# Kernel tuning notes

Measured on AMD Instinct MI355X. Metric: run time of the kernel, lower is better.

Reference implementation:

```python
import jax, jax.numpy as jnp
import numpy as np

B, S, D, H, F, E, TOPK, W = 1, 4096, 768, 12, 3072, 7, 2, 256  # W = one-sided window


def _layer_norm(x, g, b, eps=1e-5):
    m = jnp.mean(x, -1, keepdims=True)
    v = jnp.var(x, -1, keepdims=True)
    return (x - m) * jax.lax.rsqrt(v + eps) * g + b


def _sliding_attn(x, Wq, bq, Wk, bk, Wv, bv):
    # Longformer sliding-window attention, chunked (no dense SxS matrix).
    Bx, Sx, Dx = x.shape
    Dh = Dx // H
    def proj(Wm, bm):
        return (x @ Wm + bm).reshape(Bx, Sx, H, Dh).transpose(0, 2, 1, 3)  # [B,H,S,Dh]
    q = proj(Wq, bq) * (1.0 / np.sqrt(Dh))
    k = proj(Wk, bk)
    v = proj(Wv, bv)
    nc = Sx // W
    kp = jnp.pad(k, ((0, 0), (0, 0), (W, W), (0, 0)))
    vp = jnp.pad(v, ((0, 0), (0, 0), (W, W), (0, 0)))
    # each query chunk of W tokens sees a 3W key window
    idx = (jnp.arange(nc) * W)[:, None] + jnp.arange(3 * W)[None, :]  # [nc,3W]
    kc = kp[:, :, idx]  # [B,H,nc,3W,Dh]
    vc = vp[:, :, idx]
    qc = q.reshape(Bx, H, nc, W, Dh)
    scores = jnp.einsum('bhcqd,bhckd->bhcqk', qc, kc)  # [B,H,nc,W,3W]
    qi = jnp.arange(W)[:, None]
    ki = jnp.arange(3 * W)[None, :]
    band = (ki >= qi) & (ki <= qi + 2 * W)  # |key_pos - query_pos| <= W
    pos = (jnp.arange(nc) * W)[:, None, None] + ki[None] - W  # global key pos
    valid = band[None] & (pos >= 0) & (pos < Sx)  # [nc,W,3W]
    scores = jnp.where(valid[None, None], scores, -1e9)
    probs = jax.nn.softmax(scores, axis=-1)
    out = jnp.einsum('bhcqk,bhckd->bhcqd', probs, vc)
    return out.reshape(Bx, H, Sx, Dh).transpose(0, 2, 1, 3).reshape(Bx, Sx, Dx)


def setup_inputs() -> dict:
    key = jax.random.key(0)
    ks = jax.random.split(key, 16)
    sc = 0.02
    rn = lambda k, shp: jax.random.normal(k, shp, jnp.float32) * sc
    return {
        'hidden_states': jax.random.normal(ks[0], (B, S, D), jnp.float32),
        'Wq': rn(ks[1], (D, D)), 'bq': jnp.zeros((D,), jnp.float32),
        'Wk': rn(ks[2], (D, D)), 'bk': jnp.zeros((D,), jnp.float32),
        'Wv': rn(ks[3], (D, D)), 'bv': jnp.zeros((D,), jnp.float32),
        'Wo': rn(ks[4], (D, D)), 'bo': jnp.zeros((D,), jnp.float32),
        'ln1_g': jnp.ones((D,), jnp.float32), 'ln1_b': jnp.zeros((D,), jnp.float32),
        'gate_W': rn(ks[5], (D, E)), 'gate_b': jnp.zeros((E,), jnp.float32),
        'W1e': rn(ks[6], (E, D, F)), 'b1e': jnp.zeros((E, F), jnp.float32),
        'W2e': rn(ks[7], (E, F, D)), 'b2e': jnp.zeros((E, D), jnp.float32),
        'Wd': rn(ks[8], (D, D)), 'bd': jnp.zeros((D,), jnp.float32),
        'ln2_g': jnp.ones((D,), jnp.float32), 'ln2_b': jnp.zeros((D,), jnp.float32),
    }


def reference(hidden_states, Wq, bq, Wk, bk, Wv, bv, Wo, bo, ln1_g, ln1_b,
              gate_W, gate_b, W1e, b1e, W2e, b2e, Wd, bd, ln2_g, ln2_b):
    # attention + SelfOutput (dense + residual + LN); dropout = identity (eval)
    attn = _sliding_attn(hidden_states, Wq, bq, Wk, bk, Wv, bv)
    attention_output = _layer_norm(attn @ Wo + bo + hidden_states, ln1_g, ln1_b)
    # MoE feed-forward: dense all-experts compute, top-k masked softmax gate
    gate_logits = attention_output @ gate_W + gate_b  # [B,S,E]
    topv, topi = jax.lax.top_k(gate_logits, TOPK)
    # softmax over (-inf scatter of topk) == softmax over topk values scattered back
    sw = jax.nn.softmax(topv, axis=-1)  # [B,S,k]
    gate_weights = jnp.einsum('bske,bsk->bse',
                              jax.nn.one_hot(topi, E, dtype=attention_output.dtype), sw)
    h = jax.nn.gelu(jnp.einsum('bsd,edf->bsef', attention_output, W1e) + b1e,
                    approximate=False)  # [B,S,E,F]
    eo = jnp.einsum('bsef,efd->bsed', h, W2e) + b2e  # [B,S,E,D]
    moe = jnp.einsum('bsed,bse->bsd', eo, gate_weights)
    ffn = moe @ Wd + bd
    layer_output = _layer_norm(ffn + attention_output, ln2_g, ln2_b)
    return layer_output, gate_weights
```

## Files before the change

### kernel.cpp

```cpp
#include <hip/hip_runtime.h>
#include <math.h>

#define S_LEN 4096
#define DMODEL 768
#define NHEADS 12
#define DH 64
#define FDIM 3072
#define NEXP 7
#define NPAIR (2*S_LEN)
#define MAXTILES 40

typedef _Float16 f16x8 __attribute__((ext_vector_type(8)));
typedef float f32x4 __attribute__((ext_vector_type(4)));

__device__ __forceinline__ unsigned short f2h(float f){
  union { _Float16 h; unsigned short u; } v; v.h = (_Float16)f; return v.u;
}
__device__ __forceinline__ float gelu_f(float x){
  return 0.5f * x * (1.0f + erff(x * 0.7071067811865475f));
}
__device__ __forceinline__ f32x4 mfma16(f16x8 a, f16x8 b, f32x4 c){
  return __builtin_amdgcn_mfma_f32_16x16x32_f16(a, b, c, 0, 0, 0);
}
__device__ __forceinline__ void glds16(const void* g, void* l){
  __builtin_amdgcn_global_load_lds((const __attribute__((address_space(1))) unsigned*)g,
                                   (__attribute__((address_space(3))) unsigned*)l, 16, 0, 0);
}

__global__ __launch_bounds__(256) void split_kernel(const float* __restrict__ in,
    unsigned short* __restrict__ out, int n){
  int i = blockIdx.x*256 + threadIdx.x;
  if (i >= n) return;
  out[i] = f2h(in[i]);
}

__global__ __launch_bounds__(256) void transp_kernel(const float* __restrict__ in,
    unsigned short* __restrict__ out,
    int R, int C, long inStride, long outStride){
  const float* ip = in + (long)blockIdx.z * inStride;
  long ob = (long)blockIdx.z * outStride;
  __shared__ float tile[32][33];
  int c0 = blockIdx.x*32, r0 = blockIdx.y*32;
  int tx = threadIdx.x, ty = threadIdx.y;
  for (int i = ty; i < 32; i += 8)
    tile[i][tx] = ip[(long)(r0+i)*C + c0 + tx];
  __syncthreads();
  int t  = tx + ty*32;
  int sx = t & 15;
  int sc = t >> 4;
  #pragma unroll
  for (int j = 0; j < 2; j++){
    int cc = sc + j*16;
    float v0 = tile[sx*2][cc], v1 = tile[sx*2+1][cc];
    long oidx = ob + (long)(c0+cc)*R + r0 + sx*2;
    unsigned uh = (unsigned)f2h(v0) | ((unsigned)f2h(v1) << 16);
    *(unsigned*)(out + oidx) = uh;
  }
}

struct GemmP {
  const unsigned short* A;
  const unsigned short* B;
  int M, N, K;
  const float* bias;  const float* bias2; const float* bias3;
  const float* resid;
  float* outF;
  unsigned short* outBF;
  unsigned short *qh,*kh,*vth;
  const int* pair_token;
  const float* pair_w;
  const int* cnt;
  const int* offs;
  const int* tile_e;
  const int* tile_m;
  const int* ntiles;
};

template<int MODE>
__global__ __launch_bounds__(256, 2) void gemm_bt(GemmP p){
  const int tid  = threadIdx.x;
  const int lane = tid & 63;
  const int wave = tid >> 6;
  const int quad = lane >> 4;
  const int ln   = lane & 15;
  const int wr = wave >> 1, wc = wave & 1;
  const int bn0 = blockIdx.x * 128;
  const int bm0 = blockIdx.y * 128;
  const int K = p.K;

  long aoff[2]; long boff[2]; int koff[2];
  #pragma unroll
  for (int j = 0; j < 2; j++){
    int c = tid + j*256;
    int row = c >> 2;
    koff[j] = (c & 3) * 8;
    aoff[j] = (long)(bm0 + row) * K;
    boff[j] = (long)(bn0 + row) * K;
  }

  __shared__ __align__(16) unsigned short As[2][128*32];
  __shared__ __align__(16) unsigned short Bs[2][128*32];

  auto stage = [&](int k0, int buf){
    #pragma unroll
    for (int j = 0; j < 2; j++){
      int c = tid + j*256;
      glds16(p.A + aoff[j] + k0 + koff[j], &As[buf][c*8]);
      glds16(p.B + boff[j] + k0 + koff[j], &Bs[buf][c*8]);
    }
  };

  f32x4 zero4 = {0.f, 0.f, 0.f, 0.f};
  f32x4 acc[4][4];
  #pragma unroll
  for (int i = 0; i < 4; i++)
    #pragma unroll
    for (int j = 0; j < 4; j++) acc[i][j] = zero4;

  stage(0, 0);
  __syncthreads();
  int cur = 0;

  for (int k0 = 0; k0 < K; k0 += 32){
    if (k0 + 32 < K) stage(k0 + 32, cur ^ 1);
    f16x8 af[4], bfr[4];
    #pragma unroll
    for (int mt = 0; mt < 4; mt++)
      af[mt] = *(const f16x8*)&As[cur][(wr*64 + mt*16 + ln)*32 + quad*8];
    #pragma unroll
    for (int nt = 0; nt < 4; nt++)
      bfr[nt] = *(const f16x8*)&Bs[cur][(wc*64 + nt*16 + ln)*32 + quad*8];
    #pragma unroll
    for (int mt = 0; mt < 4; mt++)
      #pragma unroll
      for (int nt = 0; nt < 4; nt++)
        acc[mt][nt] = mfma16(af[mt], bfr[nt], acc[mt][nt]);
    __syncthreads();
    cur ^= 1;
  }

  #pragma unroll
  for (int mt = 0; mt < 4; mt++){
    #pragma unroll
    for (int nt = 0; nt < 4; nt++){
      #pragma unroll
      for (int r = 0; r < 4; r++){
        int gm = bm0 + wr*64 + mt*16 + quad*4 + r;
        int gn = bn0 + wc*64 + nt*16 + ln;
        float v = acc[mt][nt][r];
        if (MODE == 0){
          int which = gn >= 1536 ? 2 : (gn >= 768 ? 1 : 0);
          int nn = gn - which*768;
          int hh = nn >> 6, dh = nn & 63;
          if (which == 0){
            float q = (v + p.bias[nn]) * 0.125f;
            long o = ((long)hh*S_LEN + gm)*64 + dh;
            p.qh[o] = f2h(q);
          } else if (which == 1){
            float kv = v + p.bias2[nn];
            long o = ((long)hh*S_LEN + gm)*64 + dh;
            p.kh[o] = f2h(kv);
          } else {
            float vv = v + p.bias3[nn];
            long o = ((long)hh*64 + dh)*S_LEN + gm;
            p.vth[o] = f2h(vv);
          }
        } else if (MODE == 1 || MODE == 4){
          long i = (long)gm*DMODEL + gn;
          p.outF[i] = v + p.bias[gn] + p.resid[i];
        }
      }
    }
  }
}

template<int MODE>
__global__ __launch_bounds__(512, 4) void gemm_big(GemmP p){
  const int ty = blockIdx.y;
  if (ty >= *p.ntiles) return;
  const int e   = p.tile_e[ty];
  const int bm0 = p.tile_m[ty];

  const int tid  = threadIdx.x;
  const int lane = tid & 63;
  const int wave = tid >> 6;
  const int quad = lane >> 4;
  const int ln   = lane & 15;
  const int wr = wave >> 1, wc = wave & 1;
  const int bn0 = blockIdx.x * 128;
  const int K = p.K;

  const int eoff = p.offs[e];
  const int Mloc = p.cnt[e];
  const unsigned short* Bp = p.B + (long)e * FDIM * DMODEL;

  long aoff[2]; int koffA[2];
  #pragma unroll
  for (int j = 0; j < 2; j++){
    int c = tid + j*512;
    int row = c >> 2;
    koffA[j] = (c & 3) * 8;
    int r = bm0 + row; if (r >= Mloc) r = Mloc - 1;
    aoff[j] = (MODE == 2) ? (long)p.pair_token[eoff + r] * K : (long)(eoff + r) * K;
  }
  long boff; int koffB;
  {
    int row = tid >> 2;
    koffB = (tid & 3) * 8;
    boff = (long)(bn0 + row) * K;
  }

  __shared__ __align__(16) unsigned short As[2][256*32];
  __shared__ __align__(16) unsigned short Bs[2][128*32];

  auto stage = [&](int k0, int buf){
    #pragma unroll
    for (int j = 0; j < 2; j++){
      int c = tid + j*512;
      glds16(p.A + aoff[j] + k0 + koffA[j], &As[buf][c*8]);
    }
    glds16(Bp + boff + k0 + koffB, &Bs[buf][tid*8]);
  };

  f32x4 zero4 = {0.f, 0.f, 0.f, 0.f};
  f32x4 acc[4][4];
  #pragma unroll
  for (int i = 0; i < 4; i++)
    #pragma unroll
    for (int j = 0; j < 4; j++) acc[i][j] = zero4;

  stage(0, 0);
  __syncthreads();
  int cur = 0;

  for (int k0 = 0; k0 < K; k0 += 32){
    if (k0 + 32 < K) stage(k0 + 32, cur ^ 1);
    f16x8 af[4], bfr[4];
    #pragma unroll
    for (int mt = 0; mt < 4; mt++)
      af[mt] = *(const f16x8*)&As[cur][(wr*64 + mt*16 + ln)*32 + quad*8];
    #pragma unroll
    for (int nt = 0; nt < 4; nt++)
      bfr[nt] = *(const f16x8*)&Bs[cur][(wc*64 + nt*16 + ln)*32 + quad*8];
    #pragma unroll
    for (int mt = 0; mt < 4; mt++)
      #pragma unroll
      for (int nt = 0; nt < 4; nt++)
        acc[mt][nt] = mfma16(af[mt], bfr[nt], acc[mt][nt]);
    __syncthreads();
    cur ^= 1;
  }

  #pragma unroll
  for (int mt = 0; mt < 4; mt++){
    #pragma unroll
    for (int nt = 0; nt < 4; nt++){
      #pragma unroll
      for (int r = 0; r < 4; r++){
        int gm = bm0 + wr*64 + mt*16 + quad*4 + r;
        int gn = bn0 + wc*64 + nt*16 + ln;
        if (gm < Mloc){
          float v = acc[mt][nt][r];
          if (MODE == 2){
            v = gelu_f(v + p.bias[(long)e*FDIM + gn]);
            p.outBF[(long)(eoff + gm)*FDIM + gn] = f2h(v);
          } else {
            int pi = eoff + gm;
            p.outF[(long)pi*DMODEL + gn] = v + p.bias[(long)e*DMODEL + gn];
          }
        }
      }
    }
  }
}

__global__ __launch_bounds__(256) void attn_mfma(
    const unsigned short* __restrict__ Qh,
    const unsigned short* __restrict__ Kh,
    const unsigned short* __restrict__ Vth,
    unsigned short* __restrict__ attn_h){
  const int c = blockIdx.x, h = blockIdx.y, qb = blockIdx.z;
  const int tid = threadIdx.x;
  const int lane = tid & 63, w = tid >> 6;
  const int quad = lane >> 4, ln = lane & 15;
  const int q0 = c*256 + qb*64;
  const int qw = q0 + w*16;

  __shared__ __align__(16) unsigned short Ks[64*64];
  __shared__ __align__(16) unsigned short Vs[64*64];
  __shared__ __align__(16) unsigned short Ps[4][16*72];

  f16x8 qf[2];
  {
    long qrow = ((long)h*S_LEN + qw + ln)*64 + quad*8;
    qf[0] = *(const f16x8*)(Qh + qrow);
    qf[1] = *(const f16x8*)(Qh + qrow + 32);
  }

  float m_s[4], l_s[4];
  f32x4 Oc[4];
  f32x4 z4 = {0.f,0.f,0.f,0.f};
  #pragma unroll
  for (int r = 0; r < 4; r++){ m_s[r] = -1e30f; l_s[r] = 0.f; }
  #pragma unroll
  for (int nt = 0; nt < 4; nt++) Oc[nt] = z4;

  const unsigned short* KB = Kh + (long)h*S_LEN*64;
  const unsigned short* VB = Vth + (long)h*64*S_LEN;

  for (int kb = 0; kb < 12; kb++){
    const int kstart = c*256 - 256 + kb*64;
    if (kstart + 63 < 0 || kstart >= S_LEN) continue;
    if (kstart + 63 < q0 - 256 || kstart > q0 + 63 + 256) continue;
    __syncthreads();
    #pragma unroll
    for (int p2 = 0; p2 < 2; p2++){
      int idx = p2*256 + tid;
      int row = idx >> 3;
      int pc  = idx & 7;
      int lc  = pc ^ (row & 7);
      int ka = kstart + row;
      int kac = ka < 0 ? 0 : (ka > S_LEN-1 ? S_LEN-1 : ka);
      long gK = (long)kac*64 + lc*8;
      glds16(KB + gK, &Ks[idx*8]);
      int ks0 = kstart + lc*8;
      ks0 = ks0 < 0 ? 0 : (ks0 > S_LEN-8 ? S_LEN-8 : ks0);
      long gV = (long)row*S_LEN + ks0;
      glds16(VB + gV, &Vs[idx*8]);
    }
    __syncthreads();
    if (kstart + 63 < qw - 256 || kstart > qw + 15 + 256) continue;

    f32x4 Sc[4];
    #pragma unroll
    for (int nt = 0; nt < 4; nt++) Sc[nt] = z4;
    #pragma unroll
    for (int kc = 0; kc < 2; kc++){
      f16x8 bh[4];
      #pragma unroll
      for (int nt = 0; nt < 4; nt++){
        int row = nt*16 + ln;
        int o = row*64 + (((kc*4 + quad) ^ (row & 7))*8);
        bh[nt] = *(const f16x8*)&Ks[o];
      }
      #pragma unroll
      for (int nt = 0; nt < 4; nt++)
        Sc[nt] = mfma16(qf[kc], bh[nt], Sc[nt]);
    }
    bool interior = (kstart >= qw - 241) && (kstart <= qw + 193) &&
                    (kstart >= 0) && (kstart + 63 <= S_LEN - 1);
    if (!interior){
      #pragma unroll
      for (int nt = 0; nt < 4; nt++){
        int ka = kstart + nt*16 + ln;
        #pragma unroll
        for (int r = 0; r < 4; r++){
          int qa = qw + quad*4 + r;
          bool v = (ka >= 0) && (ka < S_LEN) && (ka >= qa - 256) && (ka <= qa + 256);
          if (!v) Sc[nt][r] = -3.0e38f;
        }
      }
    }
    float bm[4];
    #pragma unroll
    for (int r = 0; r < 4; r++)
      bm[r] = fmaxf(fmaxf(Sc[0][r], Sc[1][r]), fmaxf(Sc[2][r], Sc[3][r]));
    #pragma unroll
    for (int off = 1; off < 16; off <<= 1)
      #pragma unroll
      for (int r = 0; r < 4; r++) bm[r] = fmaxf(bm[r], __shfl_xor(bm[r], off));
    float al[4];
    #pragma unroll
    for (int r = 0; r < 4; r++){
      float mnew = fmaxf(m_s[r], bm[r]);
      al[r] = __expf(m_s[r] - mnew);
      m_s[r] = mnew;
    }
    float psum[4] = {0.f,0.f,0.f,0.f};
    #pragma unroll
    for (int nt = 0; nt < 4; nt++){
      #pragma unroll
      for (int r = 0; r < 4; r++){
        float pv = __expf(Sc[nt][r] - m_s[r]);
        psum[r] += pv;
        int o = (quad*4 + r)*72 + nt*16 + ln;
        Ps[w][o] = f2h(pv);
      }
    }
    #pragma unroll
    for (int off = 1; off < 16; off <<= 1)
      #pragma unroll
      for (int r = 0; r < 4; r++) psum[r] += __shfl_xor(psum[r], off);
    #pragma unroll
    for (int r = 0; r < 4; r++) l_s[r] = l_s[r]*al[r] + psum[r];
    #pragma unroll
    for (int nt = 0; nt < 4; nt++)
      #pragma unroll
      for (int r = 0; r < 4; r++) Oc[nt][r] *= al[r];
    asm volatile("s_waitcnt lgkmcnt(0)" ::: "memory");
    #pragma unroll
    for (int kc = 0; kc < 2; kc++){
      f16x8 ph = *(const f16x8*)&Ps[w][ln*72 + kc*32 + quad*8];
      #pragma unroll
      for (int nt = 0; nt < 4; nt++){
        int row = nt*16 + ln;
        int o = row*64 + (((kc*4 + quad) ^ (row & 7))*8);
        f16x8 vh = *(const f16x8*)&Vs[o];
        Oc[nt] = mfma16(ph, vh, Oc[nt]);
      }
    }
  }
  float inv[4];
  #pragma unroll
  for (int r = 0; r < 4; r++) inv[r] = 1.f / l_s[r];
  #pragma unroll
  for (int nt = 0; nt < 4; nt++){
    #pragma unroll
    for (int r = 0; r < 4; r++){
      int qa = qw + quad*4 + r;
      long o = (long)qa*DMODEL + h*64 + nt*16 + ln;
      attn_h[o] = f2h(Oc[nt][r] * inv[r]);
    }
  }
}

__global__ __launch_bounds__(256) void ln_kernel(const float* __restrict__ x,
    const float* __restrict__ g, const float* __restrict__ b,
    float* __restrict__ outF, unsigned short* __restrict__ outH){
  int s = blockIdx.x;
  const float* row = x + (long)s*DMODEL;
  int t = threadIdx.x;
  float v0 = row[t], v1 = row[t+256], v2 = row[t+512];
  float sum = v0+v1+v2;
  float sq  = v0*v0 + v1*v1 + v2*v2;
  for (int o = 32; o > 0; o >>= 1){ sum += __shfl_xor(sum, o); sq += __shfl_xor(sq, o); }
  __shared__ float s1[4], s2[4];
  int wv = t >> 6;
  if ((t & 63) == 0){ s1[wv] = sum; s2[wv] = sq; }
  __syncthreads();
  sum = s1[0]+s1[1]+s1[2]+s1[3];
  sq  = s2[0]+s2[1]+s2[2]+s2[3];
  float mean = sum * (1.0f/DMODEL);
  float var  = sq  * (1.0f/DMODEL) - mean*mean;
  float inv = rsqrtf(var + 1e-5f);
  float* orow = outF + (long)s*DMODEL;
  unsigned short* hrow = outH ? outH + (long)s*DMODEL : (unsigned short*)0;
  #pragma unroll
  for (int j = 0; j < 3; j++){
    int d = t + j*256;
    float y = (row[d] - mean) * inv * g[d] + b[d];
    orow[d] = y;
    if (hrow) hrow[d] = f2h(y);
  }
}

__global__ __launch_bounds__(64) void gate_kernel(const float* __restrict__ x,
    const float* __restrict__ gw, const float* __restrict__ gb,
    float* __restrict__ gate_out, int* __restrict__ tok_e,
    float* __restrict__ tok_w, int* __restrict__ cnt){
  int s = blockIdx.x;
  int lane = threadIdx.x;
  float acc[NEXP];
  #pragma unroll
  for (int e = 0; e < NEXP; e++) acc[e] = 0.f;
  const float* xr = x + (long)s*DMODEL;
  for (int d = lane; d < DMODEL; d += 64){
    float xv = xr[d];
    const float* wr = gw + (long)d*NEXP;
    #pragma unroll
    for (int e = 0; e < NEXP; e++) acc[e] += xv * wr[e];
  }
  #pragma unroll
  for (int e = 0; e < NEXP; e++){
    float v = acc[e];
    for (int o = 32; o > 0; o >>= 1) v += __shfl_xor(v, o);
    acc[e] = v;
  }
  if (lane == 0){
    #pragma unroll
    for (int e = 0; e < NEXP; e++) acc[e] += gb[e];
    int i0 = 0;
    for (int e = 1; e < NEXP; e++) if (acc[e] > acc[i0]) i0 = e;
    int i1 = -1;
    for (int e = 0; e < NEXP; e++) if (e != i0 && (i1 < 0 || acc[e] > acc[i1])) i1 = e;
    float e1 = expf(acc[i1] - acc[i0]);
    float inv = 1.f / (1.f + e1);
    float w0 = inv, w1 = e1 * inv;
    float* go = gate_out + (long)s*NEXP;
    #pragma unroll
    for (int e = 0; e < NEXP; e++) go[e] = 0.f;
    go[i0] = w0; go[i1] = w1;
    tok_e[s*2] = i0; tok_e[s*2+1] = i1;
    tok_w[s*2] = w0; tok_w[s*2+1] = w1;
    atomicAdd(&cnt[i0], 1);
    atomicAdd(&cnt[i1], 1);
  }
}

__global__ void scan_kernel(const int* __restrict__ cnt, int* __restrict__ offs,
                            int* __restrict__ tile_e, int* __restrict__ tile_m,
                            int* __restrict__ ntiles){
  if (threadIdx.x == 0 && blockIdx.x == 0){
    int s = 0, t = 0;
    for (int e = 0; e < NEXP; e++){
      offs[e] = s;
      for (int m0 = 0; m0 < cnt[e]; m0 += 256){
        tile_e[t] = e; tile_m[t] = m0; t++;
      }
      s += cnt[e];
    }
    *ntiles = t;
  }
}

__global__ __launch_bounds__(256) void scatter_kernel(const int* __restrict__ tok_e,
    const float* __restrict__ tok_w, const int* __restrict__ offs, int* __restrict__ fill,
    int* __restrict__ pair_token, float* __restrict__ pair_w, int* __restrict__ tok_pi){
  int t = blockIdx.x*256 + threadIdx.x;
  if (t >= S_LEN) return;
  #pragma unroll
  for (int sl = 0; sl < 2; sl++){
    int e = tok_e[t*2+sl];
    int pos = atomicAdd(&fill[e], 1);
    int pi = offs[e] + pos;
    pair_token[pi] = t;
    pair_w[pi] = tok_w[t*2+sl];
    tok_pi[t*2+sl] = pi;
  }
}

__global__ __launch_bounds__(256) void combine_kernel(const float* __restrict__ Pbuf,
    const int* __restrict__ tok_pi, const float* __restrict__ tok_w,
    unsigned short* __restrict__ moe_h){
  int t = blockIdx.x;
  int d = threadIdx.x;
  float w0 = tok_w[t*2], w1 = tok_w[t*2+1];
  long p0 = (long)tok_pi[t*2]   * DMODEL;
  long p1 = (long)tok_pi[t*2+1] * DMODEL;
  unsigned short* orow = moe_h + (long)t*DMODEL;
  #pragma unroll
  for (int j = 0; j < 3; j++){
    int dd = d + j*256;
    orow[dd] = f2h(w0*Pbuf[p0+dd] + w1*Pbuf[p1+dd]);
  }
}

extern "C" void kernel_launch(void* const* d_in, const int* in_sizes, int n_in,
                              void* d_out, int out_size, void* d_ws, size_t ws_size,
                              hipStream_t stream){
  (void)in_sizes; (void)n_in; (void)out_size; (void)ws_size;
  const float* hidden = (const float*)d_in[0];
  const float* Wq  = (const float*)d_in[1];
  const float* bq  = (const float*)d_in[2];
  const float* Wk  = (const float*)d_in[3];
  const float* bk  = (const float*)d_in[4];
  const float* Wv  = (const float*)d_in[5];
  const float* bv  = (const float*)d_in[6];
  const float* Wo  = (const float*)d_in[7];
  const float* bo  = (const float*)d_in[8];
  const float* ln1g = (const float*)d_in[9];
  const float* ln1b = (const float*)d_in[10];
  const float* gateW = (const float*)d_in[11];
  const float* gateB = (const float*)d_in[12];
  const float* W1e = (const float*)d_in[13];
  const float* b1e = (const float*)d_in[14];
  const float* W2e = (const float*)d_in[15];
  const float* b2e = (const float*)d_in[16];
  const float* Wd  = (const float*)d_in[17];
  const float* bd  = (const float*)d_in[18];
  const float* ln2g = (const float*)d_in[19];
  const float* ln2b = (const float*)d_in[20];

  float* outL = (float*)d_out;
  float* outG = outL + (size_t)S_LEN*DMODEL;

  const size_t SD = (size_t)S_LEN*DMODEL;
  char* base = (char*)d_ws;
  size_t off = 0;
  auto alloc = [&](size_t bytes)->void*{
    void* r = base + off;
    off = (off + bytes + 255) & ~(size_t)255;
    return r;
  };
  unsigned short* x_h     = (unsigned short*)alloc(SD*2);
  unsigned short* wqkv_h  = (unsigned short*)alloc((size_t)2304*768*2);
  unsigned short* wo_h    = (unsigned short*)alloc((size_t)768*768*2);
  unsigned short* wd_h    = (unsigned short*)alloc((size_t)768*768*2);
  unsigned short* w1_h    = (unsigned short*)alloc((size_t)NEXP*FDIM*DMODEL*2);
  unsigned short* w2_h    = (unsigned short*)alloc((size_t)NEXP*FDIM*DMODEL*2);
  unsigned short* q_h   = (unsigned short*)alloc(SD*2);
  unsigned short* k_h   = (unsigned short*)alloc(SD*2);
  unsigned short* vt_h  = (unsigned short*)alloc(SD*2);
  unsigned short* attn_h = (unsigned short*)alloc(SD*2);
  float* preLN1    = (float*)alloc(SD*4);
  float* attnout_f = (float*)alloc(SD*4);
  unsigned short* attnout_h = (unsigned short*)alloc(SD*2);
  int*   tok_e = (int*)alloc(2*S_LEN*4);
  float* tok_w = (float*)alloc(2*S_LEN*4);
  int*   tok_pi = (int*)alloc(2*S_LEN*4);
  int*   cnt   = (int*)alloc(32*4);
  int*   fill  = cnt + 8;
  int*   offs  = (int*)alloc(32*4);
  int*   tile_e = (int*)alloc(MAXTILES*4);
  int*   tile_m = (int*)alloc(MAXTILES*4);
  int*   ntiles = (int*)alloc(4);
  int*   pair_token = (int*)alloc(NPAIR*4);
  float* pair_w     = (float*)alloc(NPAIR*4);
  unsigned short* Hbuf = (unsigned short*)alloc((size_t)NPAIR*FDIM*2);
  float* Pbuf = (float*)alloc((size_t)NPAIR*DMODEL*4);
  unsigned short* moe_h = (unsigned short*)alloc(SD*2);
  float* preLN2 = preLN1;

  split_kernel<<<dim3((unsigned)(SD/256)), dim3(256), 0, stream>>>(hidden, x_h, (int)SD);
  transp_kernel<<<dim3(24,24,1), dim3(32,8), 0, stream>>>(Wq, wqkv_h,           DMODEL, DMODEL, 0, 0);
  transp_kernel<<<dim3(24,24,1), dim3(32,8), 0, stream>>>(Wk, wqkv_h+768*768,   DMODEL, DMODEL, 0, 0);
  transp_kernel<<<dim3(24,24,1), dim3(32,8), 0, stream>>>(Wv, wqkv_h+2*768*768, DMODEL, DMODEL, 0, 0);
  transp_kernel<<<dim3(24,24,1), dim3(32,8), 0, stream>>>(Wo, wo_h, DMODEL, DMODEL, 0, 0);
  transp_kernel<<<dim3(24,24,1), dim3(32,8), 0, stream>>>(Wd, wd_h, DMODEL, DMODEL, 0, 0);
  transp_kernel<<<dim3(96,24,NEXP), dim3(32,8), 0, stream>>>(W1e, w1_h, DMODEL, FDIM, (long)DMODEL*FDIM, (long)DMODEL*FDIM);
  transp_kernel<<<dim3(24,96,NEXP), dim3(32,8), 0, stream>>>(W2e, w2_h, FDIM, DMODEL, (long)DMODEL*FDIM, (long)DMODEL*FDIM);

  GemmP pq = {};
  pq.A = x_h; pq.B = wqkv_h;
  pq.M = S_LEN; pq.N = 2304; pq.K = DMODEL;
  pq.bias = bq; pq.bias2 = bk; pq.bias3 = bv;
  pq.qh = q_h; pq.kh = k_h; pq.vth = vt_h;
  gemm_bt<0><<<dim3(18,32,1), dim3(256), 0, stream>>>(pq);

  attn_mfma<<<dim3(16,NHEADS,4), dim3(256), 0, stream>>>(q_h, k_h, vt_h, attn_h);

  GemmP pw = {};
  pw.A = attn_h; pw.B = wo_h;
  pw.M = S_LEN; pw.N = DMODEL; pw.K = DMODEL;
  pw.bias = bo; pw.resid = hidden; pw.outF = preLN1;
  gemm_bt<1><<<dim3(6,32,1), dim3(256), 0, stream>>>(pw);

  ln_kernel<<<dim3(S_LEN), dim3(256), 0, stream>>>(preLN1, ln1g, ln1b, attnout_f, attnout_h);

  hipMemsetAsync(cnt, 0, 64, stream);

  gate_kernel<<<dim3(S_LEN), dim3(64), 0, stream>>>(attnout_f, gateW, gateB, outG, tok_e, tok_w, cnt);
  scan_kernel<<<dim3(1), dim3(64), 0, stream>>>(cnt, offs, tile_e, tile_m, ntiles);
  scatter_kernel<<<dim3(S_LEN/256), dim3(256), 0, stream>>>(tok_e, tok_w, offs, fill, pair_token, pair_w, tok_pi);

  GemmP p1 = {};
  p1.A = attnout_h; p1.B = w1_h; p1.M = S_LEN; p1.N = FDIM; p1.K = DMODEL;
  p1.bias = b1e; p1.outBF = Hbuf;
  p1.pair_token = pair_token; p1.cnt = cnt; p1.offs = offs;
  p1.tile_e = tile_e; p1.tile_m = tile_m; p1.ntiles = ntiles;
  gemm_big<2><<<dim3(24,MAXTILES), dim3(512), 0, stream>>>(p1);

  GemmP p2 = {};
  p2.A = Hbuf; p2.B = w2_h; p2.M = S_LEN; p2.N = DMODEL; p2.K = FDIM;
  p2.bias = b2e; p2.outF = Pbuf;
  p2.pair_token = pair_token; p2.pair_w = pair_w; p2.cnt = cnt; p2.offs = offs;
  p2.tile_e = tile_e; p2.tile_m = tile_m; p2.ntiles = ntiles;
  gemm_big<3><<<dim3(6,MAXTILES), dim3(512), 0, stream>>>(p2);

  combine_kernel<<<dim3(S_LEN), dim3(256), 0, stream>>>(Pbuf, tok_pi, tok_w, moe_h);
  GemmP pd = {};
  pd.A = moe_h; pd.B = wd_h; pd.M = S_LEN; pd.N = DMODEL; pd.K = DMODEL;
  pd.bias = bd; pd.resid = attnout_f; pd.outF = preLN2;
  gemm_bt<4><<<dim3(6,32,1), dim3(256), 0, stream>>>(pd);

  ln_kernel<<<dim3(S_LEN), dim3(256), 0, stream>>>(preLN2, ln2g, ln2b, outL, nullptr);
}
```

Measured before the change: 729.7 us.

## Replace atomic MoE routing with single-block histogram route kernel

Removes the memset, the global atomics in the gate kernel, and the separate scan and scatter kernels. One 256-thread block now builds per-thread expert histograms, prefix-sums them and writes the pair permutation, offsets and tile lists. The gate kernel also packs four tokens per 256-thread block. This cuts launch count and atomic contention, and makes pair ordering deterministic, but the routing work is now serialized in a single block.

```diff
diff --git a/kernel.cpp b/kernel.cpp
--- a/kernel.cpp
+++ b/kernel.cpp
@@ -454,17 +454,20 @@
   }
 }
 
-__global__ __launch_bounds__(64) void gate_kernel(const float* __restrict__ x,
+__global__ __launch_bounds__(256) void gate_kernel(const float* __restrict__ x,
     const float* __restrict__ gw, const float* __restrict__ gb,
     float* __restrict__ gate_out, int* __restrict__ tok_e,
-    float* __restrict__ tok_w, int* __restrict__ cnt){
-  int s = blockIdx.x;
-  int lane = threadIdx.x;
+    float* __restrict__ tok_w){
+  int w = threadIdx.x >> 6;
+  int lane = threadIdx.x & 63;
+  int s = blockIdx.x*4 + w;
   float acc[NEXP];
   #pragma unroll
   for (int e = 0; e < NEXP; e++) acc[e] = 0.f;
   const float* xr = x + (long)s*DMODEL;
-  for (int d = lane; d < DMODEL; d += 64){
+  #pragma unroll
+  for (int j = 0; j < DMODEL/64; j++){
+    int d = lane + j*64;
     float xv = xr[d];
     const float* wr = gw + (long)d*NEXP;
     #pragma unroll
@@ -492,40 +495,46 @@
     go[i0] = w0; go[i1] = w1;
     tok_e[s*2] = i0; tok_e[s*2+1] = i1;
     tok_w[s*2] = w0; tok_w[s*2+1] = w1;
-    atomicAdd(&cnt[i0], 1);
-    atomicAdd(&cnt[i1], 1);
-  }
-}
-
-__global__ void scan_kernel(const int* __restrict__ cnt, int* __restrict__ offs,
-                            int* __restrict__ tile_e, int* __restrict__ tile_m,
-                            int* __restrict__ ntiles){
-  if (threadIdx.x == 0 && blockIdx.x == 0){
-    int s = 0, t = 0;
-    for (int e = 0; e < NEXP; e++){
-      offs[e] = s;
-      for (int m0 = 0; m0 < cnt[e]; m0 += 256){
-        tile_e[t] = e; tile_m[t] = m0; t++;
-      }
-      s += cnt[e];
-    }
-    *ntiles = t;
-  }
-}
-
-__global__ __launch_bounds__(256) void scatter_kernel(const int* __restrict__ tok_e,
-    const float* __restrict__ tok_w, const int* __restrict__ offs, int* __restrict__ fill,
-    int* __restrict__ pair_token, float* __restrict__ pair_w, int* __restrict__ tok_pi){
-  int t = blockIdx.x*256 + threadIdx.x;
-  if (t >= S_LEN) return;
-  #pragma unroll
-  for (int sl = 0; sl < 2; sl++){
-    int e = tok_e[t*2+sl];
-    int pos = atomicAdd(&fill[e], 1);
-    int pi = offs[e] + pos;
-    pair_token[pi] = t;
-    pair_w[pi] = tok_w[t*2+sl];
-    tok_pi[t*2+sl] = pi;
+  }
+}
+
+__global__ __launch_bounds__(256) void route_kernel(const int* __restrict__ tok_e,
+    const float* __restrict__ tok_w,
+    int* __restrict__ cnt, int* __restrict__ offs,
+    int* __restrict__ pair_token, float* __restrict__ pair_w, int* __restrict__ tok_pi,
+    int* __restrict__ tile_e, int* __restrict__ tile_m, int* __restrict__ ntiles){
+  __shared__ int hist[256][NEXP];
+  __shared__ int cntS[NEXP], offsS[NEXP];
+  const int t = threadIdx.x;
+  const int CH = NPAIR/256;
+  const int base = t*CH;
+  #pragma unroll
+  for (int e = 0; e < NEXP; e++) hist[t][e] = 0;
+  for (int i = 0; i < CH; i++)
+    hist[t][tok_e[base+i]]++;
+  __syncthreads();
+  if (t < NEXP){
+    int s = 0;
+    for (int i = 0; i < 256; i++){ int v = hist[i][t]; hist[i][t] = s; s += v; }
+    cntS[t] = s;
+  }
+  __syncthreads();
+  if (t == 0){
+    int s = 0, tt = 0;
+    for (int e = 0; e < NEXP; e++){ offsS[e] = s; s += cntS[e]; }
+    for (int e = 0; e < NEXP; e++)
+      for (int m0 = 0; m0 < cntS[e]; m0 += 256){ tile_e[tt] = e; tile_m[tt] = m0; tt++; }
+    *ntiles = tt;
+    for (int e = 0; e < NEXP; e++){ cnt[e] = cntS[e]; offs[e] = offsS[e]; }
+  }
+  __syncthreads();
+  for (int i = 0; i < CH; i++){
+    int idx = base + i;
+    int e = tok_e[idx];
+    int pi = offsS[e] + hist[t][e]++;
+    pair_token[pi] = idx >> 1;
+    pair_w[pi] = tok_w[idx];
+    tok_pi[idx] = pi;
   }
 }
 
@@ -599,7 +608,6 @@
   float* tok_w = (float*)alloc(2*S_LEN*4);
   int*   tok_pi = (int*)alloc(2*S_LEN*4);
   int*   cnt   = (int*)alloc(32*4);
-  int*   fill  = cnt + 8;
   int*   offs  = (int*)alloc(32*4);
   int*   tile_e = (int*)alloc(MAXTILES*4);
   int*   tile_m = (int*)alloc(MAXTILES*4);
@@ -637,11 +645,9 @@
 
   ln_kernel<<<dim3(S_LEN), dim3(256), 0, stream>>>(preLN1, ln1g, ln1b, attnout_f, attnout_h);
 
-  hipMemsetAsync(cnt, 0, 64, stream);
-
-  gate_kernel<<<dim3(S_LEN), dim3(64), 0, stream>>>(attnout_f, gateW, gateB, outG, tok_e, tok_w, cnt);
-  scan_kernel<<<dim3(1), dim3(64), 0, stream>>>(cnt, offs, tile_e, tile_m, ntiles);
-  scatter_kernel<<<dim3(S_LEN/256), dim3(256), 0, stream>>>(tok_e, tok_w, offs, fill, pair_token, pair_w, tok_pi);
+  gate_kernel<<<dim3(S_LEN/4), dim3(256), 0, stream>>>(attnout_f, gateW, gateB, outG, tok_e, tok_w);
+  route_kernel<<<dim3(1), dim3(256), 0, stream>>>(tok_e, tok_w, cnt, offs,
+      pair_token, pair_w, tok_pi, tile_e, tile_m, ntiles);
 
   GemmP p1 = {};
   p1.A = attnout_h; p1.B = w1_h; p1.M = S_LEN; p1.N = FDIM; p1.K = DMODEL;
```

Measured after the change: 609.5 us. -16.5%, faster.
